# Kernel optimization log

Hardware: AMD Instinct MI355X
Metric: run time of the kernel (lower is better)

Reference implementation:

```python
import jax, jax.numpy as jnp
import numpy as np

K = 16  # number of nearest neighbors (init kwarg k)
EPS = 1e-12  # numerical floor inside sqrt


def setup_inputs() -> dict:
    key = jax.random.key(0)
    k1, k2, k3, k4 = jax.random.split(key, 4)
    B, N, D_FEAT, D_OUT = 4, 4096, 64, 128
    coords = jax.random.normal(k1, (B, N, 3), dtype=jnp.float32)
    features = jax.random.normal(k2, (B, D_FEAT, N), dtype=jnp.float32)
    # Shared_MLP: Conv2d(10 -> d_out, kernel 1x1) == dense over channel dim
    W = jax.random.normal(k3, (D_OUT, 10), dtype=jnp.float32) * (1.0 / np.sqrt(10.0))
    b = jax.random.normal(k4, (D_OUT,), dtype=jnp.float32) * 0.01
    return {"coords": coords, "features": features, "W": W, "b": b}


def reference(coords, features, W, b):
    # coords: [B, N, 3]; features: [B, d, N]; W: [d_out, 10]; b: [d_out]
    B, N, _ = coords.shape
    d_feat = features.shape[1]

    # --- KNN via squared pairwise distances (per batch) ---
    sq = jnp.sum(coords * coords, axis=-1)  # [B, N]
    d2 = sq[:, :, None] + sq[:, None, :] - 2.0 * jnp.einsum(
        'bnc,bmc->bnm', coords, coords)  # [B, N, N]
    d2 = jnp.maximum(d2, 0.0)
    neg_d2, idx = jax.lax.top_k(-d2, K)  # [B, N, K] (includes self, dist 0)
    knn_dist = jnp.sqrt(jnp.maximum(-neg_d2, EPS))  # [B, N, K]

    # --- gather neighbor coords ---
    p_j = jax.vmap(lambda c, i: c[i])(coords, idx)  # [B, N, K, 3]
    p_i = jnp.broadcast_to(coords[:, :, None, :], p_j.shape)  # [B, N, K, 3]

    # --- relative position encoding: [p_i, p_j, p_i - p_j, dist] -> 10 ch ---
    enc = jnp.concatenate(
        [p_i, p_j, p_i - p_j, knn_dist[..., None]], axis=-1)  # [B, N, K, 10]

    # --- 1x1 conv MLP over channels ---
    r = jnp.einsum('bnkc,oc->bonk', enc, W) + b[None, :, None, None]
    # r: [B, d_out, N, K]

    # --- concat features (broadcast over neighbor dim) along channels ---
    feats = jnp.broadcast_to(features[:, :, :, None], (B, d_feat, N, K))
    return jnp.concatenate([r, feats], axis=1)  # [B, d_out + d, N, K]
```

## Files before the change

kernel.cpp:

```cpp
#include <hip/hip_runtime.h>
#include <math.h>

#define N_PTS 4096
#define KNN   16
#define DFEAT 64
#define DOUT  128
#define CTOT  192

__device__ __forceinline__ float d2_of(float4 ci, float4 cj) {
    float dot = ci.x * cj.x + ci.y * cj.y + ci.z * cj.z;
    float d2  = (ci.w + cj.w) - 2.0f * dot;
    return fmaxf(d2, 0.0f);
}

__global__ void knn_kernel(const float* __restrict__ coords,
                           int* __restrict__ idx_ws,
                           float* __restrict__ dist_ws)
{
    __shared__ float4 cs[N_PTS];
    const int tid = threadIdx.x;
    const int q0  = blockIdx.x * 16;
    const int b   = q0 >> 12;

    const float* cb = coords + (size_t)b * N_PTS * 3;
    for (int j = tid; j < N_PTS; j += 1024) {
        float x = cb[j * 3 + 0], y = cb[j * 3 + 1], z = cb[j * 3 + 2];
        float sq = x * x + y * y + z * z;
        cs[j] = make_float4(x, y, z, sq);
    }
    __syncthreads();

    const int wave = tid >> 6;
    const int lane = tid & 63;
    const int q = q0 + wave;
    const int n = q & (N_PTS - 1);

    const float4 ci = cs[n];

    const float SENT  = 3.0e38f;
    const int   JSENT = 0x7fffffff;
    float m1 = SENT, m2 = SENT;
    int   j1 = JSENT, j2 = JSENT;

    for (int t = 0; t < 64; ++t) {
        int   j = (t << 6) + lane;
        float d = d2_of(ci, cs[j]);
        bool lt1 = (d < m1);
        bool lt2 = (d < m2);
        float nm2 = lt1 ? m1 : (lt2 ? d : m2);
        int   nj2 = lt1 ? j1 : (lt2 ? j : j2);
        m1 = lt1 ? d : m1;  j1 = lt1 ? j : j1;
        m2 = nm2;           j2 = nj2;
    }

    unsigned long long taken = 0ull;
    float outd = 0.0f; int outj = 0;

    for (int k = 0; k < KNN; ++k) {
        float rm = m1; int rj = j1;
        #pragma unroll
        for (int s = 1; s < 64; s <<= 1) {
            float om = __shfl_xor(rm, s);
            int   oj = __shfl_xor(rj, s);
            if (om < rm || (om == rm && oj < rj)) { rm = om; rj = oj; }
        }
        if (lane == k) { outd = rm; outj = rj; }

        if (j1 == rj) {
            taken |= 1ull << (j1 >> 6);
            m1 = m2; j1 = j2;
            m2 = SENT; j2 = JSENT;
        }

        if (j1 == JSENT && k < KNN - 1) {
            m1 = SENT; m2 = SENT; j1 = JSENT; j2 = JSENT;
            for (int t = 0; t < 64; ++t) {
                if ((taken >> t) & 1ull) continue;
                int   j = (t << 6) + lane;
                float d = d2_of(ci, cs[j]);
                bool lt1 = (d < m1);
                bool lt2 = (d < m2);
                float nm2 = lt1 ? m1 : (lt2 ? d : m2);
                int   nj2 = lt1 ? j1 : (lt2 ? j : j2);
                m1 = lt1 ? d : m1;  j1 = lt1 ? j : j1;
                m2 = nm2;           j2 = nj2;
            }
        }
    }

    if (lane < KNN) {
        idx_ws[q * KNN + lane]  = outj;
        dist_ws[q * KNN + lane] = sqrtf(fmaxf(outd, 1e-12f));
    }
}

__global__ __launch_bounds__(256) void out_kernel(
    const float* __restrict__ coords, const float* __restrict__ features,
    const float* __restrict__ W, const float* __restrict__ bias,
    const int* __restrict__ idx_ws, const float* __restrict__ dist_ws,
    float* __restrict__ out)
{
    __shared__ float Ws[DOUT * 12];
    __shared__ float bs[DOUT];
    const int tid = threadIdx.x;
    for (int i = tid; i < DOUT * 12; i += 256) {
        int o = i / 12, t = i - o * 12;
        Ws[i] = (t < 10) ? W[o * 10 + t] : 0.0f;
    }
    if (tid < DOUT) bs[tid] = bias[tid];
    __syncthreads();

    const int g = blockIdx.x * 256 + tid;
    const int k = g & (KNN - 1);
    const int n = (g >> 4) & (N_PTS - 1);
    const int b = g >> 16;

    const float* cb = coords + (size_t)b * N_PTS * 3;
    const int   nb   = idx_ws[g];
    const float dist = dist_ws[g];
    const float pix = cb[n * 3 + 0],  piy = cb[n * 3 + 1],  piz = cb[n * 3 + 2];
    const float pjx = cb[nb * 3 + 0], pjy = cb[nb * 3 + 1], pjz = cb[nb * 3 + 2];

    const float e0 = pix, e1 = piy, e2 = piz;
    const float e3 = pjx, e4 = pjy, e5 = pjz;
    const float e6 = pix - pjx, e7 = piy - pjy, e8 = piz - pjz, e9 = dist;

    float* outb = out + (size_t)b * CTOT * N_PTS * KNN + (size_t)n * KNN + k;
    #pragma unroll 4
    for (int o = 0; o < DOUT; ++o) {
        const float4 w0 = *reinterpret_cast<const float4*>(&Ws[o * 12 + 0]);
        const float4 w1 = *reinterpret_cast<const float4*>(&Ws[o * 12 + 4]);
        const float2 w2 = *reinterpret_cast<const float2*>(&Ws[o * 12 + 8]);
        float acc = bs[o]
            + e0 * w0.x + e1 * w0.y + e2 * w0.z + e3 * w0.w
            + e4 * w1.x + e5 * w1.y + e6 * w1.z + e7 * w1.w
            + e8 * w2.x + e9 * w2.y;
        outb[(size_t)o * (N_PTS * KNN)] = acc;
    }

    const float* fb = features + (size_t)b * DFEAT * N_PTS + n;
    float* outf = outb + (size_t)DOUT * (N_PTS * KNN);
    #pragma unroll 4
    for (int f = 0; f < DFEAT; ++f) {
        outf[(size_t)f * (N_PTS * KNN)] = fb[(size_t)f * N_PTS];
    }
}

extern "C" void kernel_launch(void* const* d_in, const int* in_sizes, int n_in,
                              void* d_out, int out_size, void* d_ws, size_t ws_size,
                              hipStream_t stream) {
    (void)n_in; (void)out_size; (void)ws_size;
    const float* coords   = (const float*)d_in[0];
    const float* features = (const float*)d_in[1];
    const float* W        = (const float*)d_in[2];
    const float* bias     = (const float*)d_in[3];
    float* out = (float*)d_out;

    const int B  = in_sizes[0] / (N_PTS * 3);
    const int nq = B * N_PTS;

    int*   idx_ws  = (int*)d_ws;
    float* dist_ws = (float*)((char*)d_ws + (size_t)nq * KNN * sizeof(int));

    knn_kernel<<<nq / 16, 1024, 0, stream>>>(coords, idx_ws, dist_ws);
    out_kernel<<<(nq * KNN) / 256, 256, 0, stream>>>(
        coords, features, W, bias, idx_ws, dist_ws, out);
}
```

Before: 332.9 us.

## Split waves into two queries, pack distance/index keys, keep top-4 per lane

The KNN kernel now handles two queries per wave, 32 lanes each, so each block covers 32 queries and the grid is half as large. Distance and index are packed into one 64-bit key, so comparisons and shuffle reductions act on a single value. Each lane keeps a top-4 list instead of a top-2, which should make full rescans of its candidates rarer. In exchange, each lane scans 128 candidates instead of 64, and 64-bit compares and shuffles cost more instructions.

Measured after the change: 305.8 us. 1.09x faster.

```diff
diff --git a/kernel.cpp b/kernel.cpp
--- a/kernel.cpp
+++ b/kernel.cpp
@@ -7,90 +7,100 @@
 #define DOUT  128
 #define CTOT  192
 
-__device__ __forceinline__ float d2_of(float4 ci, float4 cj) {
+#define QPB   32
+#define LPQ   32
+
+__device__ __forceinline__ unsigned long long key_of(float4 ci, float4 cj, int j) {
     float dot = ci.x * cj.x + ci.y * cj.y + ci.z * cj.z;
-    float d2  = (ci.w + cj.w) - 2.0f * dot;
-    return fmaxf(d2, 0.0f);
+    float d2  = fmaxf((ci.w + cj.w) - 2.0f * dot, 0.0f);
+    return ((unsigned long long)__float_as_uint(d2) << 32) | (unsigned)j;
 }
 
-__global__ void knn_kernel(const float* __restrict__ coords,
-                           int* __restrict__ idx_ws,
-                           float* __restrict__ dist_ws)
+#define INSERT4(kk)                                   \
+    do {                                              \
+        bool c1 = (kk) < k1, c2 = (kk) < k2;          \
+        bool c3 = (kk) < k3, c4 = (kk) < k4;          \
+        k4 = c3 ? k3 : (c4 ? (kk) : k4);              \
+        k3 = c2 ? k2 : (c3 ? (kk) : k3);              \
+        k2 = c1 ? k1 : (c2 ? (kk) : k2);              \
+        k1 = c1 ? (kk) : k1;                          \
+    } while (0)
+
+__global__ __launch_bounds__(1024) void knn_kernel(
+    const float* __restrict__ coords,
+    int* __restrict__ idx_ws,
+    float* __restrict__ dist_ws)
 {
     __shared__ float4 cs[N_PTS];
     const int tid = threadIdx.x;
-    const int q0  = blockIdx.x * 16;
+    const int q0  = blockIdx.x * QPB;
     const int b   = q0 >> 12;
 
     const float* cb = coords + (size_t)b * N_PTS * 3;
     for (int j = tid; j < N_PTS; j += 1024) {
         float x = cb[j * 3 + 0], y = cb[j * 3 + 1], z = cb[j * 3 + 2];
-        float sq = x * x + y * y + z * z;
-        cs[j] = make_float4(x, y, z, sq);
+        cs[j] = make_float4(x, y, z, x * x + y * y + z * z);
     }
     __syncthreads();
 
     const int wave = tid >> 6;
     const int lane = tid & 63;
-    const int q = q0 + wave;
-    const int n = q & (N_PTS - 1);
+    const int half = lane >> 5;
+    const int hl   = lane & 31;
+    const int q    = q0 + wave * 2 + half;
+    const int n    = q & (N_PTS - 1);
 
     const float4 ci = cs[n];
 
-    const float SENT  = 3.0e38f;
-    const int   JSENT = 0x7fffffff;
-    float m1 = SENT, m2 = SENT;
-    int   j1 = JSENT, j2 = JSENT;
+    const unsigned long long KSENT = 0xFFFFFFFFFFFFFFFFull;
+    unsigned long long k1 = KSENT, k2 = KSENT, k3 = KSENT, k4 = KSENT;
 
-    for (int t = 0; t < 64; ++t) {
-        int   j = (t << 6) + lane;
-        float d = d2_of(ci, cs[j]);
-        bool lt1 = (d < m1);
-        bool lt2 = (d < m2);
-        float nm2 = lt1 ? m1 : (lt2 ? d : m2);
-        int   nj2 = lt1 ? j1 : (lt2 ? j : j2);
-        m1 = lt1 ? d : m1;  j1 = lt1 ? j : j1;
-        m2 = nm2;           j2 = nj2;
+    for (int t = 0; t < 128; ++t) {
+        int j = (t << 5) + hl;
+        unsigned long long kk = key_of(ci, cs[j], j);
+        INSERT4(kk);
     }
 
-    unsigned long long taken = 0ull;
-    float outd = 0.0f; int outj = 0;
+    unsigned long long tak0 = 0ull, tak1 = 0ull;
+    unsigned long long outKey = 0ull;
 
     for (int k = 0; k < KNN; ++k) {
-        float rm = m1; int rj = j1;
+        unsigned long long rk = k1;
         #pragma unroll
-        for (int s = 1; s < 64; s <<= 1) {
-            float om = __shfl_xor(rm, s);
-            int   oj = __shfl_xor(rj, s);
-            if (om < rm || (om == rm && oj < rj)) { rm = om; rj = oj; }
+        for (int s = 1; s < LPQ; s <<= 1) {
+            unsigned long long o = __shfl_xor(rk, s);
+            if (o < rk) rk = o;
         }
-        if (lane == k) { outd = rm; outj = rj; }
+        if (hl == k) outKey = rk;
 
-        if (j1 == rj) {
-            taken |= 1ull << (j1 >> 6);
-            m1 = m2; j1 = j2;
-            m2 = SENT; j2 = JSENT;
+        if (k1 == rk) {
+            int t = (int)(rk & 0xFFFFFFFFull) >> 5;
+            if (t < 64) tak0 |= 1ull << t;
+            else        tak1 |= 1ull << (t - 64);
+            k1 = k2; k2 = k3; k3 = k4; k4 = KSENT;
         }
 
-        if (j1 == JSENT && k < KNN - 1) {
-            m1 = SENT; m2 = SENT; j1 = JSENT; j2 = JSENT;
+        if (k1 == KSENT && k < KNN - 1) {
+            k2 = KSENT; k3 = KSENT; k4 = KSENT;
             for (int t = 0; t < 64; ++t) {
-                if ((taken >> t) & 1ull) continue;
-                int   j = (t << 6) + lane;
-                float d = d2_of(ci, cs[j]);
-                bool lt1 = (d < m1);
-                bool lt2 = (d < m2);
-                float nm2 = lt1 ? m1 : (lt2 ? d : m2);
-                int   nj2 = lt1 ? j1 : (lt2 ? j : j2);
-                m1 = lt1 ? d : m1;  j1 = lt1 ? j : j1;
-                m2 = nm2;           j2 = nj2;
+                if ((tak0 >> t) & 1ull) continue;
+                int j = (t << 5) + hl;
+                unsigned long long kk = key_of(ci, cs[j], j);
+                INSERT4(kk);
+            }
+            for (int t = 64; t < 128; ++t) {
+                if ((tak1 >> (t - 64)) & 1ull) continue;
+                int j = (t << 5) + hl;
+                unsigned long long kk = key_of(ci, cs[j], j);
+                INSERT4(kk);
             }
         }
     }
 
-    if (lane < KNN) {
-        idx_ws[q * KNN + lane]  = outj;
-        dist_ws[q * KNN + lane] = sqrtf(fmaxf(outd, 1e-12f));
+    if (hl < KNN) {
+        float d2 = __uint_as_float((unsigned)(outKey >> 32));
+        idx_ws[q * KNN + hl]  = (int)(outKey & 0xFFFFFFFFull);
+        dist_ws[q * KNN + hl] = sqrtf(fmaxf(d2, 1e-12f));
     }
 }
 
@@ -162,7 +172,7 @@
     int*   idx_ws  = (int*)d_ws;
     float* dist_ws = (float*)((char*)d_ws + (size_t)nq * KNN * sizeof(int));
 
-    knn_kernel<<<nq / 16, 1024, 0, stream>>>(coords, idx_ws, dist_ws);
+    knn_kernel<<<nq / QPB, 1024, 0, stream>>>(coords, idx_ws, dist_ws);
     out_kernel<<<(nq * KNN) / 256, 256, 0, stream>>>(
         coords, features, W, bias, idx_ws, dist_ws, out);
 }
```
